# Kernel tuning notes

Hardware: AMD Instinct MI355X
Metric: run time of the kernel (lower is better)

Reference implementation:

```python
import jax, jax.numpy as jnp
import numpy as np
import math

N = 100000      # num nodes
D = 5           # fixed degree per node (<=5 -> exact Shapley enumeration path)
F_IN = 128
F_OUT = 128


def _subset_coeffs(d):
    """Exact Shapley subset-enumeration coefficients for a node with d neighbors.
    For subset S (mask m_k over neighbor slots, |S|=s):
      marginal = (sum_S + x_i)/(s+1) - (sum_S/s if s>0 else 0)   [since mean_S]
      weight   = s! (d-s)! / (d+1)!
    contrib = sum_k w_k*marginal_k = einsum(sum_S, c1) + x_i * sum(c2)
    """
    k = np.arange(2 ** d)
    masks = ((k[:, None] >> np.arange(d)) & 1).astype(np.float32)  # [2^d, d]
    s = masks.sum(axis=1)
    fact = np.vectorize(math.factorial)
    w = (fact(s.astype(np.int64)) * fact((d - s).astype(np.int64))
         / math.factorial(d + 1)).astype(np.float32)
    c1 = np.where(s > 0, w * (1.0 / (s + 1.0) - 1.0 / np.maximum(s, 1.0)), 0.0).astype(np.float32)
    c2 = (w / (s + 1.0)).astype(np.float32)
    return jnp.asarray(masks), jnp.asarray(c1), jnp.asarray(float(c2.sum()))


def setup_inputs() -> dict:
    key = jax.random.key(0)
    k1, k2, k3 = jax.random.split(key, 3)
    x = jax.random.normal(k1, (N, F_IN), dtype=jnp.float32)
    # fixed-degree graph: node i owns edges [i*D, (i+1)*D); row sorted
    row = jnp.repeat(jnp.arange(N, dtype=jnp.int32), D)
    col = jax.random.randint(k2, (N * D,), 0, N, dtype=jnp.int32)
    edge_index = jnp.stack([row, col])  # [2, N*D]
    W = jax.random.normal(k3, (F_OUT, F_IN), dtype=jnp.float32) / np.float32(np.sqrt(F_IN))
    return {"x": x, "edge_index": edge_index, "W": W}


def reference(x, edge_index, W):
    n = x.shape[0]
    col = edge_index[1]
    d = col.shape[0] // n
    nbrs = col.reshape(n, d)          # neighbors of node i (row is sorted, fixed degree)
    xn = x[nbrs]                      # [n, d, f] gathered neighbor features
    masks, c1, c2_sum = _subset_coeffs(d)
    # per-subset neighbor-feature sums: [n, 2^d, f]
    sum_S = jnp.einsum('kd,ndf->nkf', masks, xn)
    contrib = jnp.einsum('nkf,k->nf', sum_S, c1) + x * c2_sum
    shapley = x + contrib             # x_i + Shapley contribution
    out = jax.nn.relu(shapley @ W.T)  # Linear(bias=False) + relu
    return out
```

## Files before the change

### kernel.cpp

```cpp
#include <hip/hip_runtime.h>
#include <hip/hip_bf16.h>

typedef __attribute__((ext_vector_type(8))) short short8;
typedef __attribute__((ext_vector_type(4))) float f32x4;

#define DEG 5
#define FDIM 128
#define MT 64
#define NTHR 256
#define LROW 136

__device__ __forceinline__ short f2bf(float f) {
    unsigned u = __builtin_bit_cast(unsigned, f);
    unsigned r = (u + 0x7fffu + ((u >> 16) & 1u)) >> 16;
    return (short)(r & 0xffffu);
}

__global__ __launch_bounds__(256) void prep_w_kernel(
    const float* __restrict__ W, short* __restrict__ wswz)
{
    int t = blockIdx.x * 256 + threadIdx.x;
    int frag = t >> 6;
    int lane = t & 63;
    int tt = frag >> 2;
    int kk = frag & 3;
    int lr = lane & 15;
    int lg = lane >> 4;
    const float4* wp = reinterpret_cast<const float4*>(W + (tt * 16 + lr) * FDIM + kk * 32 + lg * 8);
    float4 w0 = wp[0], w1 = wp[1];
    short8 v;
    v[0] = f2bf(w0.x); v[1] = f2bf(w0.y); v[2] = f2bf(w0.z); v[3] = f2bf(w0.w);
    v[4] = f2bf(w1.x); v[5] = f2bf(w1.y); v[6] = f2bf(w1.z); v[7] = f2bf(w1.w);
    *reinterpret_cast<short8*>(wswz + (size_t)t * 8) = v;
}

__global__ __launch_bounds__(NTHR) void shapley_gnn_kernel(
    const float* __restrict__ x,
    const int* __restrict__ col,
    const short* __restrict__ wswz,
    float* __restrict__ out,
    int n)
{
    __shared__ short sS[MT * LROW];
    __shared__ int sIdx[MT * DEG];

    const int tid = threadIdx.x;
    const int base = blockIdx.x * MT;

    for (int i = tid; i < MT * DEG; i += NTHR) {
        int e = base * DEG + i;
        sIdx[i] = (e < n * DEG) ? col[e] : 0;
    }
    __syncthreads();

    const float CSELF = 1.4083333333333334f;
    const float ALPHA = -0.04833333333333333f;

    for (int t = tid; t < MT * 16; t += NTHR) {
        int m = t >> 4;
        int c = t & 15;
        int node = base + m;
        float a0, a1, a2, a3, a4, a5, a6, a7;
        if (node < n) {
            const float4* xp = reinterpret_cast<const float4*>(x + (size_t)node * FDIM + c * 8);
            float4 s0 = xp[0], s1 = xp[1];
            a0 = CSELF * s0.x; a1 = CSELF * s0.y; a2 = CSELF * s0.z; a3 = CSELF * s0.w;
            a4 = CSELF * s1.x; a5 = CSELF * s1.y; a6 = CSELF * s1.z; a7 = CSELF * s1.w;
            #pragma unroll
            for (int j = 0; j < DEG; ++j) {
                int nb = sIdx[m * DEG + j];
                const float4* np = reinterpret_cast<const float4*>(x + (size_t)nb * FDIM + c * 8);
                float4 b0 = np[0], b1 = np[1];
                a0 += ALPHA * b0.x; a1 += ALPHA * b0.y; a2 += ALPHA * b0.z; a3 += ALPHA * b0.w;
                a4 += ALPHA * b1.x; a5 += ALPHA * b1.y; a6 += ALPHA * b1.z; a7 += ALPHA * b1.w;
            }
        } else {
            a0 = a1 = a2 = a3 = a4 = a5 = a6 = a7 = 0.f;
        }
        short8 v;
        v[0] = f2bf(a0); v[1] = f2bf(a1); v[2] = f2bf(a2); v[3] = f2bf(a3);
        v[4] = f2bf(a4); v[5] = f2bf(a5); v[6] = f2bf(a6); v[7] = f2bf(a7);
        *reinterpret_cast<short8*>(&sS[m * LROW + c * 8]) = v;
    }
    __syncthreads();

    const int wave = tid >> 6;
    const int lane = tid & 63;
    const int lr = lane & 15;
    const int lg = lane >> 4;

    short8 afrag[4];
    const short* arow = &sS[(wave * 16 + lr) * LROW];
    #pragma unroll
    for (int kk = 0; kk < 4; ++kk)
        afrag[kk] = *reinterpret_cast<const short8*>(arow + kk * 32 + lg * 8);

    f32x4 acc[8];
    #pragma unroll
    for (int t = 0; t < 8; ++t) acc[t] = (f32x4){0.f, 0.f, 0.f, 0.f};

    #pragma unroll
    for (int t = 0; t < 8; ++t) {
        #pragma unroll
        for (int kk = 0; kk < 4; ++kk) {
            short8 bfrag = *reinterpret_cast<const short8*>(
                wswz + (((size_t)(t * 4 + kk) * 64 + lane) * 8));
            acc[t] = __builtin_amdgcn_mfma_f32_16x16x32_bf16(afrag[kk], bfrag, acc[t], 0, 0, 0);
        }
    }

    #pragma unroll
    for (int t = 0; t < 8; ++t) {
        #pragma unroll
        for (int i = 0; i < 4; ++i) {
            int nrow = base + wave * 16 + lg * 4 + i;
            if (nrow < n) {
                float v = acc[t][i];
                out[(size_t)nrow * FDIM + t * 16 + lr] = v > 0.f ? v : 0.f;
            }
        }
    }
}

extern "C" void kernel_launch(void* const* d_in, const int* in_sizes, int n_in,
                              void* d_out, int out_size, void* d_ws, size_t ws_size,
                              hipStream_t stream) {
    const float* x  = (const float*)d_in[0];
    const int* ei   = (const int*)d_in[1];
    const float* W  = (const float*)d_in[2];
    float* out      = (float*)d_out;
    short* wswz     = (short*)d_ws;

    int n = in_sizes[0] / FDIM;
    const int* col = ei + (size_t)n * DEG;

    hipLaunchKernelGGL(prep_w_kernel, dim3(8), dim3(256), 0, stream, W, wswz);

    int blocks = (n + MT - 1) / MT;
    hipLaunchKernelGGL(shapley_gnn_kernel, dim3(blocks), dim3(NTHR), 0, stream,
                       x, col, wswz, out, n);
}
```

Before: 60.75 us.

## Apply linear layer before neighbor aggregation and gather bf16 projected rows

Because the linear layer distributes over the neighbor sum, the work is split into two kernels. The first computes Y = x·Wᵀ per node and stores it in bf16 in the workspace. The second gathers the self and neighbor rows of Y, applies the Shapley coefficients, then ReLU. Gathered rows are bf16 instead of fp32, which halves the bytes of the random neighbor gathers. The cost is an extra kernel launch, a full write and re-read of the intermediate Y, and an added bf16 rounding of Y before the sum. The new path runs only when the workspace is large enough; otherwise the original fused kernel is used.

```diff
diff --git a/kernel.cpp b/kernel.cpp
--- a/kernel.cpp
+++ b/kernel.cpp
@@ -10,10 +10,16 @@
 #define NTHR 256
 #define LROW 136
 
+#define CSELF 1.4083333333333334f
+#define ALPHA (-0.04833333333333333f)
+
 __device__ __forceinline__ short f2bf(float f) {
     unsigned u = __builtin_bit_cast(unsigned, f);
     unsigned r = (u + 0x7fffu + ((u >> 16) & 1u)) >> 16;
     return (short)(r & 0xffffu);
+}
+__device__ __forceinline__ float bf2f(short s) {
+    return __builtin_bit_cast(float, (unsigned)((unsigned short)s) << 16);
 }
 
 __global__ __launch_bounds__(256) void prep_w_kernel(
@@ -34,6 +40,124 @@
     *reinterpret_cast<short8*>(wswz + (size_t)t * 8) = v;
 }
 
+__global__ __launch_bounds__(NTHR) void gemm_y_kernel(
+    const float* __restrict__ x,
+    const short* __restrict__ wswz,
+    short* __restrict__ Y,
+    int n)
+{
+    __shared__ short sS[MT * LROW];
+    const int tid = threadIdx.x;
+    const int base = blockIdx.x * MT;
+
+    for (int t = tid; t < MT * 16; t += NTHR) {
+        int m = t >> 4;
+        int c = t & 15;
+        int node = base + m;
+        short8 v;
+        if (node < n) {
+            const float4* xp = reinterpret_cast<const float4*>(x + (size_t)node * FDIM + c * 8);
+            float4 s0 = xp[0], s1 = xp[1];
+            v[0] = f2bf(s0.x); v[1] = f2bf(s0.y); v[2] = f2bf(s0.z); v[3] = f2bf(s0.w);
+            v[4] = f2bf(s1.x); v[5] = f2bf(s1.y); v[6] = f2bf(s1.z); v[7] = f2bf(s1.w);
+        } else {
+            v = (short8)0;
+        }
+        *reinterpret_cast<short8*>(&sS[m * LROW + c * 8]) = v;
+    }
+    __syncthreads();
+
+    const int wave = tid >> 6;
+    const int lane = tid & 63;
+    const int lr = lane & 15;
+    const int lg = lane >> 4;
+
+    short8 afrag[4];
+    const short* arow = &sS[(wave * 16 + lr) * LROW];
+    #pragma unroll
+    for (int kk = 0; kk < 4; ++kk)
+        afrag[kk] = *reinterpret_cast<const short8*>(arow + kk * 32 + lg * 8);
+    __syncthreads();
+
+    f32x4 acc[8];
+    #pragma unroll
+    for (int t = 0; t < 8; ++t) acc[t] = (f32x4){0.f, 0.f, 0.f, 0.f};
+
+    #pragma unroll
+    for (int t = 0; t < 8; ++t) {
+        #pragma unroll
+        for (int kk = 0; kk < 4; ++kk) {
+            short8 bfrag = *reinterpret_cast<const short8*>(
+                wswz + (((size_t)(t * 4 + kk) * 64 + lane) * 8));
+            acc[t] = __builtin_amdgcn_mfma_f32_16x16x32_bf16(afrag[kk], bfrag, acc[t], 0, 0, 0);
+        }
+    }
+
+    #pragma unroll
+    for (int t = 0; t < 8; ++t) {
+        #pragma unroll
+        for (int i = 0; i < 4; ++i) {
+            sS[(wave * 16 + lg * 4 + i) * LROW + t * 16 + lr] = f2bf(acc[t][i]);
+        }
+    }
+    __syncthreads();
+
+    for (int t = tid; t < MT * 16; t += NTHR) {
+        int m = t >> 4;
+        int c = t & 15;
+        if (base + m < n) {
+            *reinterpret_cast<short8*>(Y + (size_t)(base + m) * FDIM + c * 8) =
+                *reinterpret_cast<const short8*>(&sS[m * LROW + c * 8]);
+        }
+    }
+}
+
+__global__ __launch_bounds__(NTHR) void combine_kernel(
+    const short* __restrict__ Y,
+    const int* __restrict__ col,
+    float* __restrict__ out,
+    int n)
+{
+    __shared__ int sIdx[MT * DEG];
+    const int tid = threadIdx.x;
+    const int base = blockIdx.x * MT;
+
+    for (int i = tid; i < MT * DEG; i += NTHR) {
+        int e = base * DEG + i;
+        sIdx[i] = (e < n * DEG) ? col[e] : 0;
+    }
+    __syncthreads();
+
+    const int slot = tid >> 4;
+    const int c = tid & 15;
+
+    #pragma unroll
+    for (int u = 0; u < 4; ++u) {
+        int ms = u * 16 + slot;
+        int node = base + ms;
+        if (node < n) {
+            const short8 sv = *reinterpret_cast<const short8*>(Y + (size_t)node * FDIM + c * 8);
+            short8 nv[DEG];
+            #pragma unroll
+            for (int j = 0; j < DEG; ++j) {
+                int nb = sIdx[ms * DEG + j];
+                nv[j] = *reinterpret_cast<const short8*>(Y + (size_t)nb * FDIM + c * 8);
+            }
+            float r[8];
+            #pragma unroll
+            for (int k = 0; k < 8; ++k) {
+                float s = bf2f(nv[0][k]) + bf2f(nv[1][k]) + bf2f(nv[2][k])
+                        + bf2f(nv[3][k]) + bf2f(nv[4][k]);
+                float v = CSELF * bf2f(sv[k]) + ALPHA * s;
+                r[k] = v > 0.f ? v : 0.f;
+            }
+            float4* op = reinterpret_cast<float4*>(out + (size_t)node * FDIM + c * 8);
+            op[0] = (float4){r[0], r[1], r[2], r[3]};
+            op[1] = (float4){r[4], r[5], r[6], r[7]};
+        }
+    }
+}
+
 __global__ __launch_bounds__(NTHR) void shapley_gnn_kernel(
     const float* __restrict__ x,
     const int* __restrict__ col,
@@ -52,9 +176,6 @@
         sIdx[i] = (e < n * DEG) ? col[e] : 0;
     }
     __syncthreads();
-
-    const float CSELF = 1.4083333333333334f;
-    const float ALPHA = -0.04833333333333333f;
 
     for (int t = tid; t < MT * 16; t += NTHR) {
         int m = t >> 4;
@@ -129,14 +250,25 @@
     const int* ei   = (const int*)d_in[1];
     const float* W  = (const float*)d_in[2];
     float* out      = (float*)d_out;
-    short* wswz     = (short*)d_ws;
 
     int n = in_sizes[0] / FDIM;
     const int* col = ei + (size_t)n * DEG;
 
+    short* wswz = (short*)d_ws;
+    size_t y_off = 32768;
+    size_t need = y_off + (size_t)n * FDIM * sizeof(short);
+
     hipLaunchKernelGGL(prep_w_kernel, dim3(8), dim3(256), 0, stream, W, wswz);
 
     int blocks = (n + MT - 1) / MT;
-    hipLaunchKernelGGL(shapley_gnn_kernel, dim3(blocks), dim3(NTHR), 0, stream,
-                       x, col, wswz, out, n);
-}
+    if (ws_size >= need) {
+        short* Y = (short*)((char*)d_ws + y_off);
+        hipLaunchKernelGGL(gemm_y_kernel, dim3(blocks), dim3(NTHR), 0, stream,
+                           x, wswz, Y, n);
+        hipLaunchKernelGGL(combine_kernel, dim3(blocks), dim3(NTHR), 0, stream,
+                           Y, col, out, n);
+    } else {
+        hipLaunchKernelGGL(shapley_gnn_kernel, dim3(blocks), dim3(NTHR), 0, stream,
+                           x, col, wswz, out, n);
+    }
+}
```

New measurement: 58.74 us. -3.3%, faster.

## Pre-convert x to bf16 and use a persistent kernel with double-buffered register gathers

Applied to the files above, without the earlier changes.

Adds a pass that converts x to bf16 in the workspace, so the neighbor gathers move half as many bytes. The main kernel becomes persistent with 625 blocks and 32-row tiles. Each block prefetches the next tile's self and neighbor rows into registers while it computes the current tile's MFMA matmul. The trade-offs are an extra full read and write of x in the conversion pass and higher register pressure, plus extra rounding because neighbor sums are now formed from bf16 inputs. The old path is kept as a fallback when the workspace is too small.

```diff
diff --git a/kernel.cpp b/kernel.cpp
--- a/kernel.cpp
+++ b/kernel.cpp
@@ -6,14 +6,21 @@
 
 #define DEG 5
 #define FDIM 128
-#define MT 64
+#define MT 32
 #define NTHR 256
 #define LROW 136
+#define NBG 625
+
+#define CSELF 1.4083333333333334f
+#define ALPHA (-0.04833333333333333f)
 
 __device__ __forceinline__ short f2bf(float f) {
     unsigned u = __builtin_bit_cast(unsigned, f);
     unsigned r = (u + 0x7fffu + ((u >> 16) & 1u)) >> 16;
     return (short)(r & 0xffffu);
+}
+__device__ __forceinline__ float bf2f(short s) {
+    return __builtin_bit_cast(float, (unsigned)((unsigned short)s) << 16);
 }
 
 __global__ __launch_bounds__(256) void prep_w_kernel(
@@ -34,29 +41,162 @@
     *reinterpret_cast<short8*>(wswz + (size_t)t * 8) = v;
 }
 
-__global__ __launch_bounds__(NTHR) void shapley_gnn_kernel(
+__global__ __launch_bounds__(256) void conv_xb_kernel(
+    const float* __restrict__ x, short* __restrict__ xb, long total8)
+{
+    long t = (long)blockIdx.x * 256 + threadIdx.x;
+    if (t < total8) {
+        const f32x4* xp = reinterpret_cast<const f32x4*>(x + t * 8);
+        f32x4 a = xp[0], b = xp[1];
+        short8 v;
+        v[0] = f2bf(a[0]); v[1] = f2bf(a[1]); v[2] = f2bf(a[2]); v[3] = f2bf(a[3]);
+        v[4] = f2bf(b[0]); v[5] = f2bf(b[1]); v[6] = f2bf(b[2]); v[7] = f2bf(b[3]);
+        *reinterpret_cast<short8*>(xb + t * 8) = v;
+    }
+}
+
+struct SetRegs {
+    short8 self[2];
+    short8 nb[2][DEG];
+    int tbase;
+    int valid;
+};
+
+__device__ __forceinline__ void load_tile(
+    SetRegs& S, int tt, int NT,
+    const short* __restrict__ xb, const int* __restrict__ col,
+    int n, int tid)
+{
+    S.valid = (tt < NT);
+    int tb = (S.valid ? tt : 0) * MT;
+    S.tbase = tb;
+    const int c = tid & 15;
+    const int srow = tid >> 4;
+    #pragma unroll
+    for (int u = 0; u < 2; ++u) {
+        int node = tb + u * 16 + srow;
+        int nc = node < n ? node : 0;
+        S.self[u] = *reinterpret_cast<const short8*>(xb + (size_t)nc * FDIM + c * 8);
+        #pragma unroll
+        for (int j = 0; j < DEG; ++j) {
+            int nbr = col[nc * DEG + j];
+            S.nb[u][j] = *reinterpret_cast<const short8*>(xb + (size_t)nbr * FDIM + c * 8);
+        }
+    }
+}
+
+__device__ __forceinline__ void comp_tile(
+    const SetRegs& S, short* sS,
+    const short* __restrict__ wswz, float* __restrict__ out,
+    int n, int tid)
+{
+    const int c = tid & 15;
+    const int srow = tid >> 4;
+
+    #pragma unroll
+    for (int u = 0; u < 2; ++u) {
+        int row = u * 16 + srow;
+        short8 v;
+        #pragma unroll
+        for (int k = 0; k < 8; ++k) {
+            float s = bf2f(S.nb[u][0][k]) + bf2f(S.nb[u][1][k]) + bf2f(S.nb[u][2][k])
+                    + bf2f(S.nb[u][3][k]) + bf2f(S.nb[u][4][k]);
+            float vf = CSELF * bf2f(S.self[u][k]) + ALPHA * s;
+            v[k] = f2bf(vf);
+        }
+        *reinterpret_cast<short8*>(&sS[row * LROW + c * 8]) = v;
+    }
+    __syncthreads();
+
+    const int wave = tid >> 6;
+    const int lane = tid & 63;
+    const int lr = lane & 15;
+    const int lg = lane >> 4;
+    const int rt = wave & 1;
+    const int cg = wave >> 1;
+
+    short8 af[4];
+    const short* arow = &sS[(rt * 16 + lr) * LROW];
+    #pragma unroll
+    for (int kk = 0; kk < 4; ++kk)
+        af[kk] = *reinterpret_cast<const short8*>(arow + kk * 32 + lg * 8);
+    __syncthreads();
+
+    f32x4 acc[4];
+    #pragma unroll
+    for (int q = 0; q < 4; ++q) acc[q] = (f32x4){0.f, 0.f, 0.f, 0.f};
+
+    #pragma unroll
+    for (int q = 0; q < 4; ++q) {
+        int tcol = cg * 4 + q;
+        #pragma unroll
+        for (int kk = 0; kk < 4; ++kk) {
+            short8 bf = *reinterpret_cast<const short8*>(
+                wswz + (((size_t)(tcol * 4 + kk) * 64 + lane) * 8));
+            acc[q] = __builtin_amdgcn_mfma_f32_16x16x32_bf16(af[kk], bf, acc[q], 0, 0, 0);
+        }
+    }
+
+    #pragma unroll
+    for (int q = 0; q < 4; ++q) {
+        #pragma unroll
+        for (int i = 0; i < 4; ++i) {
+            int nrow = S.tbase + rt * 16 + lg * 4 + i;
+            if (nrow < n) {
+                float v = acc[q][i];
+                out[(size_t)nrow * FDIM + (cg * 4 + q) * 16 + lr] = v > 0.f ? v : 0.f;
+            }
+        }
+    }
+}
+
+__global__ __launch_bounds__(NTHR) void shapley_persistent_kernel(
+    const short* __restrict__ xb,
+    const int* __restrict__ col,
+    const short* __restrict__ wswz,
+    float* __restrict__ out,
+    int n, int NT)
+{
+    __shared__ short sS[MT * LROW];
+    const int tid = threadIdx.x;
+    const int b = blockIdx.x;
+    const int G = gridDim.x;
+
+    SetRegs A, B;
+    load_tile(A, b, NT, xb, col, n, tid);
+    int k = 0;
+    while (true) {
+        load_tile(B, b + (k + 1) * G, NT, xb, col, n, tid);
+        if (A.valid) comp_tile(A, sS, wswz, out, n, tid);
+        ++k;
+        if (b + (size_t)k * G >= (size_t)NT) break;
+        load_tile(A, b + (k + 1) * G, NT, xb, col, n, tid);
+        if (B.valid) comp_tile(B, sS, wswz, out, n, tid);
+        ++k;
+        if (b + (size_t)k * G >= (size_t)NT) break;
+    }
+}
+
+__global__ __launch_bounds__(NTHR) void shapley_fb_kernel(
     const float* __restrict__ x,
     const int* __restrict__ col,
     const short* __restrict__ wswz,
     float* __restrict__ out,
     int n)
 {
-    __shared__ short sS[MT * LROW];
-    __shared__ int sIdx[MT * DEG];
+    __shared__ short sS[64 * LROW];
+    __shared__ int sIdx[64 * DEG];
 
     const int tid = threadIdx.x;
-    const int base = blockIdx.x * MT;
-
-    for (int i = tid; i < MT * DEG; i += NTHR) {
+    const int base = blockIdx.x * 64;
+
+    for (int i = tid; i < 64 * DEG; i += NTHR) {
         int e = base * DEG + i;
         sIdx[i] = (e < n * DEG) ? col[e] : 0;
     }
     __syncthreads();
 
-    const float CSELF = 1.4083333333333334f;
-    const float ALPHA = -0.04833333333333333f;
-
-    for (int t = tid; t < MT * 16; t += NTHR) {
+    for (int t = tid; t < 64 * 16; t += NTHR) {
         int m = t >> 4;
         int c = t & 15;
         int node = base + m;
@@ -129,14 +269,29 @@
     const int* ei   = (const int*)d_in[1];
     const float* W  = (const float*)d_in[2];
     float* out      = (float*)d_out;
-    short* wswz     = (short*)d_ws;
 
     int n = in_sizes[0] / FDIM;
     const int* col = ei + (size_t)n * DEG;
 
+    short* wswz = (short*)d_ws;
+    size_t xb_off = 32768;
+    size_t need   = xb_off + (size_t)n * FDIM * sizeof(short);
+
     hipLaunchKernelGGL(prep_w_kernel, dim3(8), dim3(256), 0, stream, W, wswz);
 
-    int blocks = (n + MT - 1) / MT;
-    hipLaunchKernelGGL(shapley_gnn_kernel, dim3(blocks), dim3(NTHR), 0, stream,
-                       x, col, wswz, out, n);
-}
+    if (ws_size >= need) {
+        short* xb = (short*)((char*)d_ws + xb_off);
+        long total8 = (long)n * FDIM / 8;
+        int cblocks = (int)((total8 + 255) / 256);
+        hipLaunchKernelGGL(conv_xb_kernel, dim3(cblocks), dim3(256), 0, stream,
+                           x, xb, total8);
+        int NT = (n + MT - 1) / MT;
+        int g = NT < NBG ? NT : NBG;
+        hipLaunchKernelGGL(shapley_persistent_kernel, dim3(g), dim3(NTHR), 0, stream,
+                           xb, col, wswz, out, n, NT);
+    } else {
+        int blocks = (n + 63) / 64;
+        hipLaunchKernelGGL(shapley_fb_kernel, dim3(blocks), dim3(NTHR), 0, stream,
+                           x, col, wswz, out, n);
+    }
+}
```

Result: faster. 56.89 us (-6.4%).
